# Kernel tuning notes

Measured on AMD Instinct MI355X. Metric: run time of the kernel, lower is better.

The kernel has to match this reference:

```python
import jax, jax.numpy as jnp
import numpy as np
from functools import partial

N_NODES = 100000
IN_FEATS = 64
HIDDEN = 32
N_EDGES = 3200000


def gcn_conv(x, edge_index, W, b, num_nodes):
    """PyG GCNConv: x' = D^-1/2 (A+I) D^-1/2 (x W) + b, degrees include self-loops."""
    xw = x @ W  # [N, H]
    loop = jnp.arange(num_nodes, dtype=edge_index.dtype)
    src = jnp.concatenate([edge_index[0], loop])
    dst = jnp.concatenate([edge_index[1], loop])
    deg = jax.ops.segment_sum(jnp.ones_like(dst, dtype=xw.dtype), dst,
                              num_segments=num_nodes)  # in-degree incl. self-loop
    dinv = jnp.where(deg > 0, jax.lax.rsqrt(deg), 0.0)
    norm = dinv[src] * dinv[dst]  # [E+N]
    msg = xw[src] * norm[:, None]  # gather + scale
    out = jax.ops.segment_sum(msg, dst, num_segments=num_nodes)  # scatter-add
    return out + b


def setup_inputs() -> dict:
    key = jax.random.key(0)
    ks = jax.random.split(key, 6)
    scale = 1.0 / np.sqrt(IN_FEATS)
    return {
        "x_house": jax.random.normal(ks[0], (N_NODES, IN_FEATS), dtype=jnp.float32),
        "edge_index_near": jax.random.randint(ks[1], (2, N_EDGES), 0, N_NODES, dtype=jnp.int64)
            if jax.config.jax_enable_x64 else jax.random.randint(ks[1], (2, N_EDGES), 0, N_NODES).astype(jnp.int32),
        "edge_index_similar": jax.random.randint(ks[2], (2, N_EDGES), 0, N_NODES).astype(jnp.int32),
        "W_near": jax.random.normal(ks[3], (IN_FEATS, HIDDEN), dtype=jnp.float32) * scale,
        "b_near": jnp.zeros((HIDDEN,), dtype=jnp.float32),
        "W_similar": jax.random.normal(ks[4], (IN_FEATS, HIDDEN), dtype=jnp.float32) * scale,
        "b_similar": jnp.zeros((HIDDEN,), dtype=jnp.float32),
        "W_lin": jax.random.normal(ks[5], (HIDDEN, 1), dtype=jnp.float32) * (1.0 / np.sqrt(HIDDEN)),
        "b_lin": jnp.zeros((1,), dtype=jnp.float32),
    }


def reference(x_house, edge_index_near, edge_index_similar,
              W_near, b_near, W_similar, b_similar, W_lin, b_lin):
    # HeteroConv with aggr='sum': sum of per-edge-type GCNConv outputs on 'house'
    h = (gcn_conv(x_house, edge_index_near, W_near, b_near, N_NODES)
         + gcn_conv(x_house, edge_index_similar, W_similar, b_similar, N_NODES))
    h = jax.nn.relu(h)
    # dropout is identity at inference (training=False)
    out = h @ W_lin + b_lin  # [N, 1]
    return out.squeeze(-1)
```

## Files before the change

### kernel.cpp

```cpp
#include <hip/hip_runtime.h>
#include <hip/hip_fp16.h>


#define SLICES 256
#define BSZ    256
#define NB_MAX 800
#define CAP2   9216
#define PCH    4096
#define LDSPAD 33
#define FXS    65536.0f
#define FXSI   (1.0f / 65536.0f)

__global__ __launch_bounds__(512)
void place_kernel(const int* __restrict__ ei_n, const int* __restrict__ ei_s,
                  int* __restrict__ goff, unsigned int* __restrict__ codes,
                  int En, int Es, int nb) {
    __shared__ unsigned stg[PCH];
    __shared__ unsigned stg2[PCH];
    __shared__ int histT[NB_MAX];
    __shared__ int cur[NB_MAX];
    __shared__ int histC[NB_MAX];
    __shared__ int baseC[NB_MAX];
    __shared__ int gbC[NB_MAX];
    __shared__ int h2[NB_MAX / 2];
    const int t = threadIdx.x;
    const int type = blockIdx.y;
    const int* __restrict__ ei = type ? ei_s : ei_n;
    const int E = type ? Es : En;
    int per = ((E + SLICES - 1) / SLICES + 7) & ~7;
    const int e0 = blockIdx.x * per;
    const int e1 = min(e0 + per, E);
    const int P = (nb + 1) >> 1;

    for (int b = t; b < nb; b += 512) histT[b] = 0;
    __syncthreads();

    for (int c0 = e0; c0 < e1; c0 += PCH) {
        const int i = c0 + t * 8;
        int nv = e1 - i; nv = nv < 0 ? 0 : (nv > 8 ? 8 : nv);
        if (nv == 8) {
            int4 dA = *(const int4*)(ei + E + i), dB = *(const int4*)(ei + E + i + 4);
            atomicAdd(&histT[dA.x >> 7], 1);
            atomicAdd(&histT[dA.y >> 7], 1);
            atomicAdd(&histT[dA.z >> 7], 1);
            atomicAdd(&histT[dA.w >> 7], 1);
            atomicAdd(&histT[dB.x >> 7], 1);
            atomicAdd(&histT[dB.y >> 7], 1);
            atomicAdd(&histT[dB.z >> 7], 1);
            atomicAdd(&histT[dB.w >> 7], 1);
        } else {
            for (int j = 0; j < nv; ++j) atomicAdd(&histT[ei[E + i + j] >> 7], 1);
        }
    }
    __syncthreads();

    for (int b = t; b < nb; b += 512) {
        int c = histT[b];
        cur[b] = b * CAP2 + (c ? atomicAdd(&goff[b], c) : 0);
    }
    __syncthreads();

    for (int c0 = e0; c0 < e1; c0 += PCH) {
        for (int b = t; b < nb; b += 512) histC[b] = 0;
        __syncthreads();

        const int i = c0 + t * 8;
        int nv = e1 - i; nv = nv < 0 ? 0 : (nv > 8 ? 8 : nv);
        unsigned cd[8]; int bb[8], rk[8];
        if (nv == 8) {
            int4 sA = *(const int4*)(ei + i),     sB = *(const int4*)(ei + i + 4);
            int4 dA = *(const int4*)(ei + E + i), dB = *(const int4*)(ei + E + i + 4);
            int ss[8] = {sA.x, sA.y, sA.z, sA.w, sB.x, sB.y, sB.z, sB.w};
            int dd[8] = {dA.x, dA.y, dA.z, dA.w, dB.x, dB.y, dB.z, dB.w};
#pragma unroll
            for (int j = 0; j < 8; ++j) {
                bb[j] = dd[j] >> 7;
                cd[j] = ((unsigned)(2 * (dd[j] & 127) + type) << 18)
                      | (unsigned)(2 * ss[j] + type);
            }
        } else {
            for (int j = 0; j < nv; ++j) {
                int sv = ei[i + j], dv = ei[E + i + j];
                bb[j] = dv >> 7;
                cd[j] = ((unsigned)(2 * (dv & 127) + type) << 18)
                      | (unsigned)(2 * sv + type);
            }
        }
#pragma unroll
        for (int j = 0; j < 8; ++j)
            if (j < nv) rk[j] = atomicAdd(&histC[bb[j]], 1);
        __syncthreads();

        if (t < P) {
            int a = histC[2 * t];
            int b2 = (2 * t + 1 < nb) ? histC[2 * t + 1] : 0;
            h2[t] = a + b2;
        }
        __syncthreads();
        for (int o = 1; o < P; o <<= 1) {
            int v = (t < P && t >= o) ? h2[t - o] : 0;
            __syncthreads();
            if (t < P) h2[t] += v;
            __syncthreads();
        }
        if (t < P) {
            int a = histC[2 * t];
            int b2 = (2 * t + 1 < nb) ? histC[2 * t + 1] : 0;
            int inc = h2[t];
            baseC[2 * t] = inc - a - b2;
            if (2 * t + 1 < nb) baseC[2 * t + 1] = inc - b2;
        }
        for (int b = t; b < nb; b += 512) gbC[b] = cur[b];
        __syncthreads();

#pragma unroll
        for (int j = 0; j < 8; ++j)
            if (j < nv) {
                int p = baseC[bb[j]] + rk[j];
                stg[p] = cd[j];
                stg2[p] = (unsigned)(gbC[bb[j]] + rk[j]);
            }
        __syncthreads();

        for (int b = t; b < nb; b += 512) cur[b] = gbC[b] + histC[b];
        const int tot = min(PCH, e1 - c0);
        for (int j = t; j < tot; j += 512)
            codes[stg2[j]] = stg[j];
        __syncthreads();
    }
}

__global__ __launch_bounds__(256)
void dcxw_kernel(const unsigned int* __restrict__ codes, const int* __restrict__ goff,
                 const float* __restrict__ x,
                 const float* __restrict__ Wn, const float* __restrict__ Ws,
                 int* __restrict__ cnt, __half2* __restrict__ xws, int N, int M) {
    __shared__ float wtn[32 * 64];
    __shared__ float wts[32 * 64];
    __shared__ int dcnt[BSZ];
    const int t = threadIdx.x;
    dcnt[t] = 0;
    for (int i = t; i < 64 * 32; i += 256) {
        int k = i >> 5, h = i & 31;
        wtn[h * 64 + k] = Wn[i];
        wts[h * 64 + k] = Ws[i];
    }
    __syncthreads();

    const int b = blockIdx.x;
    const int base = b * CAP2;
    const int end = base + goff[b];
    const int t0 = base + ((end - base) & ~3);
    for (int e = base + t * 4; e < t0; e += 256 * 4) {
        uint4 c = *(const uint4*)(codes + e);
        atomicAdd(&dcnt[c.x >> 18], 1);
        atomicAdd(&dcnt[c.y >> 18], 1);
        atomicAdd(&dcnt[c.z >> 18], 1);
        atomicAdd(&dcnt[c.w >> 18], 1);
    }
    if (t < end - t0) atomicAdd(&dcnt[codes[t0 + t] >> 18], 1);
    __syncthreads();

    const int vnode = b * BSZ + t;
    if (vnode < M) cnt[vnode] = dcnt[t];

    const int p = t >> 1, half = t & 1;
    const int node = b * 128 + p;
    if (node >= N) return;

    float xr[64];
    const float4* x4 = (const float4*)(x + (size_t)node * 64);
#pragma unroll
    for (int q = 0; q < 16; ++q) {
        float4 v = x4[q];
        xr[4 * q] = v.x; xr[4 * q + 1] = v.y; xr[4 * q + 2] = v.z; xr[4 * q + 3] = v.w;
    }
    float dn = rsqrtf((float)dcnt[2 * p] + 1.0f);
    float ds = rsqrtf((float)dcnt[2 * p + 1] + 1.0f);

    unsigned pn[8], ps[8];
#pragma unroll
    for (int s2i = 0; s2i < 8; ++s2i) {
        const int s2 = half * 8 + s2i;
        float a0n = 0.f, a1n = 0.f, a0s = 0.f, a1s = 0.f;
#pragma unroll
        for (int q = 0; q < 16; ++q) {
            float4 w0n = *(const float4*)&wtn[(2 * s2) * 64 + 4 * q];
            float4 w1n = *(const float4*)&wtn[(2 * s2 + 1) * 64 + 4 * q];
            float4 w0s = *(const float4*)&wts[(2 * s2) * 64 + 4 * q];
            float4 w1s = *(const float4*)&wts[(2 * s2 + 1) * 64 + 4 * q];
            float x0 = xr[4 * q], x1 = xr[4 * q + 1], x2 = xr[4 * q + 2], x3 = xr[4 * q + 3];
            a0n += x0 * w0n.x + x1 * w0n.y + x2 * w0n.z + x3 * w0n.w;
            a1n += x0 * w1n.x + x1 * w1n.y + x2 * w1n.z + x3 * w1n.w;
            a0s += x0 * w0s.x + x1 * w0s.y + x2 * w0s.z + x3 * w0s.w;
            a1s += x0 * w1s.x + x1 * w1s.y + x2 * w1s.z + x3 * w1s.w;
        }
        __half2 hn = __floats2half2_rn(a0n * dn, a1n * dn);
        __half2 hs = __floats2half2_rn(a0s * ds, a1s * ds);
        pn[s2i] = *(unsigned*)&hn;
        ps[s2i] = *(unsigned*)&hs;
    }
    uint4* on = (uint4*)(xws + (size_t)(2 * node) * 16 + half * 8);
    uint4* os = (uint4*)(xws + (size_t)(2 * node + 1) * 16 + half * 8);
    on[0] = make_uint4(pn[0], pn[1], pn[2], pn[3]);
    on[1] = make_uint4(pn[4], pn[5], pn[6], pn[7]);
    os[0] = make_uint4(ps[0], ps[1], ps[2], ps[3]);
    os[1] = make_uint4(ps[4], ps[5], ps[6], ps[7]);
}

__global__ __launch_bounds__(512)
void gather_kernel(const unsigned int* __restrict__ codes, const int* __restrict__ goff,
                   const __half2* __restrict__ xws, const int* __restrict__ cnt,
                   const float* __restrict__ b_n, const float* __restrict__ b_s,
                   const float* __restrict__ W_lin, const float* __restrict__ b_lin,
                   float* __restrict__ out, int N) {
    __shared__ int facc[BSZ * LDSPAD];
    for (int i = threadIdx.x; i < BSZ * LDSPAD; i += 512) facc[i] = 0;
    __syncthreads();
    const int b = blockIdx.x;
    const int base = b * CAP2;
    const int end = base + goff[b];
    const int sl = threadIdx.x & 15;
    const int grp = threadIdx.x >> 4;

#define GA(cc) xws[(size_t)((cc) & 0x3FFFFu) * 16 + sl]
#define ACC_EDGE(cc, ww) do {                                                \
        float2 f_ = __half22float2(ww);                                      \
        int r_ = (int)((cc) >> 18) * LDSPAD + sl;                            \
        atomicAdd(&facc[r_],      __float2int_rn(f_.x * FXS));               \
        atomicAdd(&facc[r_ + 16], __float2int_rn(f_.y * FXS));               \
    } while (0)

    const int t0 = base + ((end - base) & ~15);
    for (int e = base + grp * 16; e < t0; e += 32 * 16) {
        uint4 c0 = *(const uint4*)(codes + e);
        uint4 c1 = *(const uint4*)(codes + e + 4);
        uint4 c2 = *(const uint4*)(codes + e + 8);
        uint4 c3 = *(const uint4*)(codes + e + 12);
        __half2 w0 = GA(c0.x), w1 = GA(c0.y), w2 = GA(c0.z), w3 = GA(c0.w);
        __half2 w4 = GA(c1.x), w5 = GA(c1.y), w6 = GA(c1.z), w7 = GA(c1.w);
        __half2 w8 = GA(c2.x), w9 = GA(c2.y), wA = GA(c2.z), wB = GA(c2.w);
        __half2 wC = GA(c3.x), wD = GA(c3.y), wE = GA(c3.z), wF = GA(c3.w);
        ACC_EDGE(c0.x, w0); ACC_EDGE(c0.y, w1); ACC_EDGE(c0.z, w2); ACC_EDGE(c0.w, w3);
        ACC_EDGE(c1.x, w4); ACC_EDGE(c1.y, w5); ACC_EDGE(c1.z, w6); ACC_EDGE(c1.w, w7);
        ACC_EDGE(c2.x, w8); ACC_EDGE(c2.y, w9); ACC_EDGE(c2.z, wA); ACC_EDGE(c2.w, wB);
        ACC_EDGE(c3.x, wC); ACC_EDGE(c3.y, wD); ACC_EDGE(c3.z, wE); ACC_EDGE(c3.w, wF);
    }
    for (int e = t0 + grp; e < end; e += 32) {
        unsigned c = codes[e];
        __half2 w = GA(c);
        ACC_EDGE(c, w);
    }
#undef ACC_EDGE
#undef GA

    __syncthreads();
    const float bn0 = b_n[2 * sl], bn1 = b_n[2 * sl + 1];
    const float bs0 = b_s[2 * sl], bs1 = b_s[2 * sl + 1];
    const float wl0 = W_lin[2 * sl], wl1 = W_lin[2 * sl + 1];
    const float bl  = b_lin[0];
    for (int p = grp; p < 128; p += 32) {
        int node = b * 128 + p;
        if (node >= N) break;
        int rn = (2 * p) * LDSPAD, rs = rn + LDSPAD;
        float anx = (float)facc[rn + sl] * FXSI, any_ = (float)facc[rn + 16 + sl] * FXSI;
        float asx = (float)facc[rs + sl] * FXSI, asy  = (float)facc[rs + 16 + sl] * FXSI;
        float2 ns = __half22float2(xws[(size_t)(2 * node) * 16 + sl]);
        float2 ss = __half22float2(xws[(size_t)(2 * node + 1) * 16 + sl]);
        float dn  = rsqrtf((float)cnt[2 * node] + 1.0f);
        float dsv = rsqrtf((float)cnt[2 * node + 1] + 1.0f);
        float h0 = (anx + ns.x) * dn + bn0 + (asx + ss.x) * dsv + bs0;
        float h1 = (any_ + ns.y) * dn + bn1 + (asy + ss.y) * dsv + bs1;
        float pr = fmaxf(h0, 0.f) * wl0 + fmaxf(h1, 0.f) * wl1;
#pragma unroll
        for (int off = 8; off > 0; off >>= 1) pr += __shfl_xor(pr, off, 16);
        if (sl == 0) out[node] = pr + bl;
    }
}

extern "C" void kernel_launch(void* const* d_in, const int* in_sizes, int n_in,
                              void* d_out, int out_size, void* d_ws, size_t ws_size,
                              hipStream_t stream) {
    const float* x     = (const float*)d_in[0];
    const int*   ei_n  = (const int*)d_in[1];
    const int*   ei_s  = (const int*)d_in[2];
    const float* W_n   = (const float*)d_in[3];
    const float* b_n   = (const float*)d_in[4];
    const float* W_s   = (const float*)d_in[5];
    const float* b_s   = (const float*)d_in[6];
    const float* W_lin = (const float*)d_in[7];
    const float* b_lin = (const float*)d_in[8];
    float* out = (float*)d_out;

    const int N  = in_sizes[0] / 64;
    const int En = in_sizes[1] / 2;
    const int Es = in_sizes[2] / 2;
    const int M  = 2 * N;
    const int nb = (M + BSZ - 1) / BSZ;

    int* goff = (int*)d_ws;
    int* cnt  = goff + 1024;
    uintptr_t pc = (uintptr_t)(cnt + M);
    pc = (pc + 15) & ~(uintptr_t)15;
    unsigned int* codes = (unsigned int*)pc;
    __half2* xws = (__half2*)(codes + (size_t)nb * CAP2);

    hipMemsetAsync(goff, 0, (size_t)nb * sizeof(int), stream);

    place_kernel<<<dim3(SLICES, 2), 512, 0, stream>>>(ei_n, ei_s, goff, codes,
                                                      En, Es, nb);
    dcxw_kernel<<<nb, 256, 0, stream>>>(codes, goff, x, W_n, W_s, cnt, xws, N, M);
    gather_kernel<<<nb, 512, 0, stream>>>(codes, goff, xws, cnt,
                                          b_n, b_s, W_lin, b_lin, out, N);
}
```

Measured before the change: 293.9 us.

## Use wave-shuffle scan in place kernel and restructure xW kernel to one node per thread

The barrier-heavy Hillis-Steele prefix scan over bin counts in place_kernel becomes a wave-level shuffle scan plus a small per-wave sum combine, which removes many __syncthreads per chunk. The xW/degree kernel now handles two buckets per block and one node per thread, reading transposed weights from global memory (prepared once by a new init kernel that also replaces the memset) instead of staging them in LDS per block. The scan change cuts synchronisation cost, while the xW change trades LDS weight reads for cached global reads and higher register use.

```diff
diff --git a/kernel.cpp b/kernel.cpp
--- a/kernel.cpp
+++ b/kernel.cpp
@@ -10,6 +10,19 @@
 #define LDSPAD 33
 #define FXS    65536.0f
 #define FXSI   (1.0f / 65536.0f)
+
+__global__ __launch_bounds__(512)
+void init_kernel(const float* __restrict__ Wn, const float* __restrict__ Ws,
+                 int* __restrict__ goff, float* __restrict__ wtn,
+                 float* __restrict__ wts, int nb) {
+    const int t = threadIdx.x;
+    for (int b = t; b < nb; b += 512) goff[b] = 0;
+    for (int i = t; i < 64 * 32; i += 512) {
+        int k = i >> 5, h = i & 31;
+        wtn[h * 64 + k] = Wn[i];
+        wts[h * 64 + k] = Ws[i];
+    }
+}
 
 __global__ __launch_bounds__(512)
 void place_kernel(const int* __restrict__ ei_n, const int* __restrict__ ei_s,
@@ -22,15 +35,15 @@
     __shared__ int histC[NB_MAX];
     __shared__ int baseC[NB_MAX];
     __shared__ int gbC[NB_MAX];
-    __shared__ int h2[NB_MAX / 2];
+    __shared__ int wsum[8];
     const int t = threadIdx.x;
+    const int wid = t >> 6, lane = t & 63;
     const int type = blockIdx.y;
     const int* __restrict__ ei = type ? ei_s : ei_n;
     const int E = type ? Es : En;
     int per = ((E + SLICES - 1) / SLICES + 7) & ~7;
     const int e0 = blockIdx.x * per;
     const int e1 = min(e0 + per, E);
-    const int P = (nb + 1) >> 1;
 
     for (int b = t; b < nb; b += 512) histT[b] = 0;
     __syncthreads();
@@ -58,12 +71,10 @@
         int c = histT[b];
         cur[b] = b * CAP2 + (c ? atomicAdd(&goff[b], c) : 0);
     }
+    for (int b = t; b < nb; b += 512) histC[b] = 0;
     __syncthreads();
 
     for (int c0 = e0; c0 < e1; c0 += PCH) {
-        for (int b = t; b < nb; b += 512) histC[b] = 0;
-        __syncthreads();
-
         const int i = c0 + t * 8;
         int nv = e1 - i; nv = nv < 0 ? 0 : (nv > 8 ? 8 : nv);
         unsigned cd[8]; int bb[8], rk[8];
@@ -91,26 +102,29 @@
             if (j < nv) rk[j] = atomicAdd(&histC[bb[j]], 1);
         __syncthreads();
 
-        if (t < P) {
-            int a = histC[2 * t];
-            int b2 = (2 * t + 1 < nb) ? histC[2 * t + 1] : 0;
-            h2[t] = a + b2;
-        }
-        __syncthreads();
-        for (int o = 1; o < P; o <<= 1) {
-            int v = (t < P && t >= o) ? h2[t - o] : 0;
-            __syncthreads();
-            if (t < P) h2[t] += v;
-            __syncthreads();
-        }
-        if (t < P) {
-            int a = histC[2 * t];
-            int b2 = (2 * t + 1 < nb) ? histC[2 * t + 1] : 0;
-            int inc = h2[t];
-            baseC[2 * t] = inc - a - b2;
-            if (2 * t + 1 < nb) baseC[2 * t + 1] = inc - b2;
-        }
-        for (int b = t; b < nb; b += 512) gbC[b] = cur[b];
+        const int i0 = wid * 128 + lane, i1 = i0 + 64;
+        int v0 = (i0 < nb) ? histC[i0] : 0;
+        int v1 = (i1 < nb) ? histC[i1] : 0;
+        int x0 = v0;
+#pragma unroll
+        for (int o = 1; o < 64; o <<= 1) { int n = __shfl_up(x0, o, 64); if (lane >= o) x0 += n; }
+        int tot0 = __shfl(x0, 63, 64);
+        int x1 = v1;
+#pragma unroll
+        for (int o = 1; o < 64; o <<= 1) { int n = __shfl_up(x1, o, 64); if (lane >= o) x1 += n; }
+        int tot1 = __shfl(x1, 63, 64);
+        if (lane == 0) wsum[wid] = tot0 + tot1;
+        for (int b = t; b < nb; b += 512) {
+            int c = histC[b], g = cur[b];
+            gbC[b] = g;
+            cur[b] = g + c;
+        }
+        __syncthreads();
+        int woff = 0;
+#pragma unroll
+        for (int k = 0; k < 8; ++k) woff += (k < wid) ? wsum[k] : 0;
+        if (i0 < nb) baseC[i0] = woff + (x0 - v0);
+        if (i1 < nb) baseC[i1] = woff + tot0 + (x1 - v1);
         __syncthreads();
 
 #pragma unroll
@@ -122,10 +136,10 @@
             }
         __syncthreads();
 
-        for (int b = t; b < nb; b += 512) cur[b] = gbC[b] + histC[b];
         const int tot = min(PCH, e1 - c0);
         for (int j = t; j < tot; j += 512)
             codes[stg2[j]] = stg[j];
+        for (int b = t; b < nb; b += 512) histC[b] = 0;
         __syncthreads();
     }
 }
@@ -133,39 +147,38 @@
 __global__ __launch_bounds__(256)
 void dcxw_kernel(const unsigned int* __restrict__ codes, const int* __restrict__ goff,
                  const float* __restrict__ x,
-                 const float* __restrict__ Wn, const float* __restrict__ Ws,
-                 int* __restrict__ cnt, __half2* __restrict__ xws, int N, int M) {
-    __shared__ float wtn[32 * 64];
-    __shared__ float wts[32 * 64];
-    __shared__ int dcnt[BSZ];
+                 const float* __restrict__ wtn, const float* __restrict__ wts,
+                 int* __restrict__ cnt, __half2* __restrict__ xws, int N, int M, int nb) {
+    __shared__ int dcnt[512];
     const int t = threadIdx.x;
     dcnt[t] = 0;
-    for (int i = t; i < 64 * 32; i += 256) {
-        int k = i >> 5, h = i & 31;
-        wtn[h * 64 + k] = Wn[i];
-        wts[h * 64 + k] = Ws[i];
-    }
-    __syncthreads();
-
-    const int b = blockIdx.x;
-    const int base = b * CAP2;
-    const int end = base + goff[b];
-    const int t0 = base + ((end - base) & ~3);
-    for (int e = base + t * 4; e < t0; e += 256 * 4) {
-        uint4 c = *(const uint4*)(codes + e);
-        atomicAdd(&dcnt[c.x >> 18], 1);
-        atomicAdd(&dcnt[c.y >> 18], 1);
-        atomicAdd(&dcnt[c.z >> 18], 1);
-        atomicAdd(&dcnt[c.w >> 18], 1);
-    }
-    if (t < end - t0) atomicAdd(&dcnt[codes[t0 + t] >> 18], 1);
-    __syncthreads();
-
-    const int vnode = b * BSZ + t;
-    if (vnode < M) cnt[vnode] = dcnt[t];
-
-    const int p = t >> 1, half = t & 1;
-    const int node = b * 128 + p;
+    dcnt[t + 256] = 0;
+    __syncthreads();
+
+    for (int bb = 0; bb < 2; ++bb) {
+        const int bidx = 2 * blockIdx.x + bb;
+        if (bidx >= nb) break;
+        const int off = bb << 8;
+        const int base = bidx * CAP2;
+        const int end = base + goff[bidx];
+        const int t0 = base + ((end - base) & ~3);
+        for (int e = base + t * 4; e < t0; e += 256 * 4) {
+            uint4 c = *(const uint4*)(codes + e);
+            atomicAdd(&dcnt[off + (c.x >> 18)], 1);
+            atomicAdd(&dcnt[off + (c.y >> 18)], 1);
+            atomicAdd(&dcnt[off + (c.z >> 18)], 1);
+            atomicAdd(&dcnt[off + (c.w >> 18)], 1);
+        }
+        if (t < end - t0) atomicAdd(&dcnt[off + (codes[t0 + t] >> 18)], 1);
+    }
+    __syncthreads();
+
+    const int v0 = blockIdx.x * 512 + t;
+    if (v0 < M) cnt[v0] = dcnt[t];
+    const int v1 = v0 + 256;
+    if (v1 < M) cnt[v1] = dcnt[t + 256];
+
+    const int node = blockIdx.x * 256 + t;
     if (node >= N) return;
 
     float xr[64];
@@ -175,20 +188,22 @@
         float4 v = x4[q];
         xr[4 * q] = v.x; xr[4 * q + 1] = v.y; xr[4 * q + 2] = v.z; xr[4 * q + 3] = v.w;
     }
-    float dn = rsqrtf((float)dcnt[2 * p] + 1.0f);
-    float ds = rsqrtf((float)dcnt[2 * p + 1] + 1.0f);
-
-    unsigned pn[8], ps[8];
-#pragma unroll
-    for (int s2i = 0; s2i < 8; ++s2i) {
-        const int s2 = half * 8 + s2i;
+    float dn = rsqrtf((float)dcnt[2 * t] + 1.0f);
+    float ds = rsqrtf((float)dcnt[2 * t + 1] + 1.0f);
+
+    const float4* wn4 = (const float4*)wtn;
+    const float4* ws4 = (const float4*)wts;
+
+    unsigned pn[16], ps[16];
+#pragma unroll
+    for (int s2 = 0; s2 < 16; ++s2) {
         float a0n = 0.f, a1n = 0.f, a0s = 0.f, a1s = 0.f;
 #pragma unroll
         for (int q = 0; q < 16; ++q) {
-            float4 w0n = *(const float4*)&wtn[(2 * s2) * 64 + 4 * q];
-            float4 w1n = *(const float4*)&wtn[(2 * s2 + 1) * 64 + 4 * q];
-            float4 w0s = *(const float4*)&wts[(2 * s2) * 64 + 4 * q];
-            float4 w1s = *(const float4*)&wts[(2 * s2 + 1) * 64 + 4 * q];
+            float4 w0n = wn4[(2 * s2) * 16 + q];
+            float4 w1n = wn4[(2 * s2 + 1) * 16 + q];
+            float4 w0s = ws4[(2 * s2) * 16 + q];
+            float4 w1s = ws4[(2 * s2 + 1) * 16 + q];
             float x0 = xr[4 * q], x1 = xr[4 * q + 1], x2 = xr[4 * q + 2], x3 = xr[4 * q + 3];
             a0n += x0 * w0n.x + x1 * w0n.y + x2 * w0n.z + x3 * w0n.w;
             a1n += x0 * w1n.x + x1 * w1n.y + x2 * w1n.z + x3 * w1n.w;
@@ -197,15 +212,16 @@
         }
         __half2 hn = __floats2half2_rn(a0n * dn, a1n * dn);
         __half2 hs = __floats2half2_rn(a0s * ds, a1s * ds);
-        pn[s2i] = *(unsigned*)&hn;
-        ps[s2i] = *(unsigned*)&hs;
-    }
-    uint4* on = (uint4*)(xws + (size_t)(2 * node) * 16 + half * 8);
-    uint4* os = (uint4*)(xws + (size_t)(2 * node + 1) * 16 + half * 8);
-    on[0] = make_uint4(pn[0], pn[1], pn[2], pn[3]);
-    on[1] = make_uint4(pn[4], pn[5], pn[6], pn[7]);
-    os[0] = make_uint4(ps[0], ps[1], ps[2], ps[3]);
-    os[1] = make_uint4(ps[4], ps[5], ps[6], ps[7]);
+        pn[s2] = *(unsigned*)&hn;
+        ps[s2] = *(unsigned*)&hs;
+    }
+    uint4* on = (uint4*)(xws + (size_t)(2 * node) * 16);
+    uint4* os = (uint4*)(xws + (size_t)(2 * node + 1) * 16);
+#pragma unroll
+    for (int q = 0; q < 4; ++q) {
+        on[q] = make_uint4(pn[4 * q], pn[4 * q + 1], pn[4 * q + 2], pn[4 * q + 3]);
+        os[q] = make_uint4(ps[4 * q], ps[4 * q + 1], ps[4 * q + 2], ps[4 * q + 3]);
+    }
 }
 
 __global__ __launch_bounds__(512)
@@ -298,18 +314,20 @@
     const int M  = 2 * N;
     const int nb = (M + BSZ - 1) / BSZ;
 
-    int* goff = (int*)d_ws;
-    int* cnt  = goff + 1024;
-    uintptr_t pc = (uintptr_t)(cnt + M);
+    int*   goff = (int*)d_ws;
+    int*   cnt  = goff + 1024;
+    float* wtn  = (float*)(cnt + M);
+    float* wts  = wtn + 2048;
+    uintptr_t pc = (uintptr_t)(wts + 2048);
     pc = (pc + 15) & ~(uintptr_t)15;
     unsigned int* codes = (unsigned int*)pc;
     __half2* xws = (__half2*)(codes + (size_t)nb * CAP2);
 
-    hipMemsetAsync(goff, 0, (size_t)nb * sizeof(int), stream);
-
+    init_kernel<<<1, 512, 0, stream>>>(W_n, W_s, goff, wtn, wts, nb);
     place_kernel<<<dim3(SLICES, 2), 512, 0, stream>>>(ei_n, ei_s, goff, codes,
                                                       En, Es, nb);
-    dcxw_kernel<<<nb, 256, 0, stream>>>(codes, goff, x, W_n, W_s, cnt, xws, N, M);
+    dcxw_kernel<<<(nb + 1) / 2, 256, 0, stream>>>(codes, goff, x, wtn, wts,
+                                                  cnt, xws, N, M, nb);
     gather_kernel<<<nb, 512, 0, stream>>>(codes, goff, xws, cnt,
                                           b_n, b_s, W_lin, b_lin, out, N);
 }
```

After: 292.2 us. About the same (-0.6%).
